# Kernel optimization log

Hardware: AMD Instinct MI355X
Metric: run time of the kernel (lower is better)

## Reference

```python
import jax, jax.numpy as jnp
import numpy as np

CHEB_K = 2  # chebyshev polynomial order (support_ks = [I, A] for cheb_k=2)


def _fc(x, w1, b1, w2, b2, w3, b3):
    # FC module: Linear -> sigmoid -> Linear -> sigmoid -> Linear
    h = jax.nn.sigmoid(x @ w1 + b1)
    h = jax.nn.sigmoid(h @ w2 + b2)
    return h @ w3 + b3


def _preprocess(adj):
    # adj: [B,N,N]; add self-loops then row-normalize
    adj = adj + jnp.eye(adj.shape[-1], dtype=adj.dtype)
    return adj / adj.sum(-1, keepdims=True)


def _gcn(x, adjs, ne, wpool, bpool):
    # x: [B,N,C], adjs: list of [B,N,N], ne: [N,E]
    # wpool: [E, 2*CHEB_K, C, O], bpool: [E, O]
    mats = []
    for A in adjs:
        ks = [jnp.broadcast_to(jnp.eye(A.shape[-1], dtype=A.dtype), A.shape), A]
        for _ in range(2, CHEB_K):
            ks.append(2.0 * jnp.matmul(A, ks[-1]) - ks[-2])
        mats.extend(ks)
    # [B,N,K,C] with K = 2*CHEB_K
    x_g = jnp.stack([jnp.einsum('bnm,bmc->bnc', S, x) for S in mats], axis=2)
    weights = jnp.einsum('nd,dkio->nkio', ne, wpool)  # [N,K,C,O]
    bias = ne @ bpool  # [N,O]
    return jnp.einsum('bnki,nkio->bno', x_g, weights) + bias


def _forward(x, state, ne0, ne1, ne2, fc1_w1, fc1_b1, fc1_w2, fc1_b2, fc1_w3, fc1_b3,
             fc2_w1, fc2_b1, fc2_w2, fc2_b2, fc2_w3, fc2_b3, gate_w, gate_b, upd_w, upd_b):
    hid = upd_w.shape[-1]
    ins = jnp.concatenate([x, state], axis=-1)  # [B,N,dim_in+hid]
    f1 = _fc(ins, fc1_w1, fc1_b1, fc1_w2, fc1_b2, fc1_w3, fc1_b3)  # [B,N,TD]
    f2 = _fc(ins, fc2_w1, fc2_b1, fc2_w2, fc2_b2, fc2_w3, fc2_b3)
    nv1 = jnp.tanh(ne0[:, None, :] * f1)  # einsum 'bd,bnd->bnd' == broadcast mul
    nv2 = jnp.tanh(ne1[:, None, :] * f2)
    adj = jnp.einsum('bnd,bmd->bnm', nv1, nv2) - jnp.einsum('bnd,bmd->bnm', nv2, nv1)
    adj1 = _preprocess(jax.nn.relu(adj))
    adj2 = _preprocess(jax.nn.relu(-jnp.swapaxes(adj, -2, -1)))
    z_r = jax.nn.sigmoid(_gcn(ins, [adj1, adj2], ne2, gate_w, gate_b))
    z, r = z_r[..., :hid], z_r[..., hid:]
    cand = jnp.concatenate([x, z * state], axis=-1)
    hc = jnp.tanh(_gcn(cand, [adj1, adj2], ne2, upd_w, upd_b))
    return r * state + (1.0 - r) * hc


def setup_inputs():
    B, N, DIN, DOUT, ED, TD = 32, 1024, 2, 64, 10, 32
    HG, MID = 16, 2  # hyperGNN_dim, middle_dim hardcoded in FC
    CIN = DIN + DOUT
    K2 = 2 * CHEB_K
    ks = jax.random.split(jax.random.key(0), 16)
    rn = lambda i, shape, s=1.0: jax.random.normal(ks[i], shape, dtype=jnp.float32) * s
    return {
        'x': rn(0, (B, N, DIN)),
        'state': rn(1, (B, N, DOUT)),
        'ne0': rn(2, (B, TD)),
        'ne1': rn(3, (B, TD)),
        'ne2': rn(4, (N, ED), 0.1),
        'fc1_w1': rn(5, (CIN, HG), 0.1), 'fc1_b1': jnp.zeros((HG,), jnp.float32),
        'fc1_w2': rn(6, (HG, MID), 0.1), 'fc1_b2': jnp.zeros((MID,), jnp.float32),
        'fc1_w3': rn(7, (MID, TD), 0.1), 'fc1_b3': jnp.zeros((TD,), jnp.float32),
        'fc2_w1': rn(8, (CIN, HG), 0.1), 'fc2_b1': jnp.zeros((HG,), jnp.float32),
        'fc2_w2': rn(9, (HG, MID), 0.1), 'fc2_b2': jnp.zeros((MID,), jnp.float32),
        'fc2_w3': rn(10, (MID, TD), 0.1), 'fc2_b3': jnp.zeros((TD,), jnp.float32),
        'gate_w': rn(11, (ED, K2, CIN, 2 * DOUT), 0.1),
        'gate_b': rn(12, (ED, 2 * DOUT), 0.1),
        'upd_w': rn(13, (ED, K2, CIN, DOUT), 0.1),
        'upd_b': rn(14, (ED, DOUT), 0.1),
    }


def reference(x, state, ne0, ne1, ne2, fc1_w1, fc1_b1, fc1_w2, fc1_b2, fc1_w3, fc1_b3,
              fc2_w1, fc2_b1, fc2_w2, fc2_b2, fc2_w3, fc2_b3, gate_w, gate_b, upd_w, upd_b):
    return _forward(x, state, ne0, ne1, ne2, fc1_w1, fc1_b1, fc1_w2, fc1_b2, fc1_w3, fc1_b3,
                    fc2_w1, fc2_b1, fc2_w2, fc2_b2, fc2_w3, fc2_b3, gate_w, gate_b, upd_w, upd_b)
```

## Files before the change

kernel.cpp:

```cpp
#include <hip/hip_runtime.h>
#include <math.h>

#define BB   32
#define NN   1024
#define DIN  2
#define DOUT 64
#define CIN  66
#define TD   32
#define ED   10
#define OG   128
#define OU   64
#define KP   160
#define XTR  80

typedef __bf16 bf16x8 __attribute__((ext_vector_type(8)));
typedef float  f32x4  __attribute__((ext_vector_type(4)));
typedef short  s16x8  __attribute__((ext_vector_type(8)));

__device__ __forceinline__ unsigned short f2b(float f) {
    __bf16 h = (__bf16)f;
    return *(unsigned short*)&h;
}

__global__ __launch_bounds__(256) void k_pre(
    const float* __restrict__ x, const float* __restrict__ state,
    const float* __restrict__ ne0, const float* __restrict__ ne1,
    const float* __restrict__ ne2,
    const float* __restrict__ w11, const float* __restrict__ b11,
    const float* __restrict__ w12, const float* __restrict__ b12,
    const float* __restrict__ w13, const float* __restrict__ b13,
    const float* __restrict__ w21, const float* __restrict__ b21,
    const float* __restrict__ w22, const float* __restrict__ b22,
    const float* __restrict__ w23, const float* __restrict__ b23,
    const float* __restrict__ gate_w, const float* __restrict__ gate_b,
    const float* __restrict__ upd_w, const float* __restrict__ upd_b,
    unsigned short* __restrict__ nv1b, unsigned short* __restrict__ nv2b,
    unsigned short* __restrict__ XT0, unsigned short* __restrict__ XT1,
    unsigned short* __restrict__ BcTg, unsigned short* __restrict__ BcTu,
    float* __restrict__ biasG, float* __restrict__ biasU)
{
    __shared__ float sw[2408];
    __shared__ unsigned short st[68*72];
    int blk = blockIdx.x;
    int t = threadIdx.x;

    if (blk < 128) {
        const int oW1 = 0, oB1 = 1056, oW2 = 1072, oB2 = 1104, oW3 = 1108, oB3 = 1172, F2 = 1204;
        for (int i = t; i < 1056; i += 256) { sw[oW1+i] = w11[i]; sw[F2+oW1+i] = w21[i]; }
        if (t < 16) { sw[oB1+t] = b11[t]; sw[F2+oB1+t] = b21[t]; }
        if (t < 32) { sw[oW2+t] = w12[t]; sw[F2+oW2+t] = w22[t]; }
        if (t < 2)  { sw[oB2+t] = b12[t]; sw[F2+oB2+t] = b22[t]; }
        if (t < 64) { sw[oW3+t] = w13[t]; sw[F2+oW3+t] = w23[t]; }
        if (t >= 64 && t < 96) { sw[oB3+t-64] = b13[t-64]; sw[F2+oB3+t-64] = b23[t-64]; }
        __syncthreads();

        int p = blk*256 + t;
        int b = p >> 10;

        float h1a[16], h1b[16];
        #pragma unroll
        for (int j = 0; j < 16; ++j) { h1a[j] = sw[oB1+j]; h1b[j] = sw[F2+oB1+j]; }
        for (int i = 0; i < CIN; ++i) {
            float v = (i < DIN) ? x[(size_t)p*DIN + i] : state[(size_t)p*DOUT + (i-DIN)];
            #pragma unroll
            for (int jq = 0; jq < 4; ++jq) {
                float4 wa = *(const float4*)&sw[oW1 + i*16 + jq*4];
                float4 wb = *(const float4*)&sw[F2 + oW1 + i*16 + jq*4];
                h1a[jq*4+0] += v*wa.x; h1a[jq*4+1] += v*wa.y;
                h1a[jq*4+2] += v*wa.z; h1a[jq*4+3] += v*wa.w;
                h1b[jq*4+0] += v*wb.x; h1b[jq*4+1] += v*wb.y;
                h1b[jq*4+2] += v*wb.z; h1b[jq*4+3] += v*wb.w;
            }
        }
        #pragma unroll
        for (int j = 0; j < 16; ++j) {
            h1a[j] = 1.f/(1.f + __expf(-h1a[j]));
            h1b[j] = 1.f/(1.f + __expf(-h1b[j]));
        }
        float h2a0 = sw[oB2+0], h2a1 = sw[oB2+1];
        float h2b0 = sw[F2+oB2+0], h2b1 = sw[F2+oB2+1];
        #pragma unroll
        for (int i = 0; i < 16; ++i) {
            h2a0 += h1a[i]*sw[oW2 + i*2 + 0];
            h2a1 += h1a[i]*sw[oW2 + i*2 + 1];
            h2b0 += h1b[i]*sw[F2+oW2 + i*2 + 0];
            h2b1 += h1b[i]*sw[F2+oW2 + i*2 + 1];
        }
        h2a0 = 1.f/(1.f + __expf(-h2a0)); h2a1 = 1.f/(1.f + __expf(-h2a1));
        h2b0 = 1.f/(1.f + __expf(-h2b0)); h2b1 = 1.f/(1.f + __expf(-h2b1));

        const float* pn0 = ne0 + b*TD;
        const float* pn1 = ne1 + b*TD;
        #pragma unroll
        for (int jq = 0; jq < 8; ++jq) {
            float4 ba  = *(const float4*)&sw[oB3 + jq*4];
            float4 wa0 = *(const float4*)&sw[oW3 + jq*4];
            float4 wa1 = *(const float4*)&sw[oW3 + 32 + jq*4];
            float4 bb2 = *(const float4*)&sw[F2+oB3 + jq*4];
            float4 wb0 = *(const float4*)&sw[F2+oW3 + jq*4];
            float4 wb1 = *(const float4*)&sw[F2+oW3 + 32 + jq*4];
            float4 n0 = *(const float4*)&pn0[jq*4];
            float4 n1 = *(const float4*)&pn1[jq*4];
            ushort4 u1, u2;
            u1.x = f2b(tanhf(n0.x*(ba.x + h2a0*wa0.x + h2a1*wa1.x)));
            u1.y = f2b(tanhf(n0.y*(ba.y + h2a0*wa0.y + h2a1*wa1.y)));
            u1.z = f2b(tanhf(n0.z*(ba.z + h2a0*wa0.z + h2a1*wa1.z)));
            u1.w = f2b(tanhf(n0.w*(ba.w + h2a0*wa0.w + h2a1*wa1.w)));
            u2.x = f2b(tanhf(n1.x*(bb2.x + h2b0*wb0.x + h2b1*wb1.x)));
            u2.y = f2b(tanhf(n1.y*(bb2.y + h2b0*wb0.y + h2b1*wb1.y)));
            u2.z = f2b(tanhf(n1.z*(bb2.z + h2b0*wb0.z + h2b1*wb1.z)));
            u2.w = f2b(tanhf(n1.w*(bb2.w + h2b0*wb0.w + h2b1*wb1.w)));
            *(ushort4*)&nv1b[(size_t)p*TD + jq*4] = u1;
            *(ushort4*)&nv2b[(size_t)p*TD + jq*4] = u2;
        }
    } else if (blk < 640) {
        int idx = blk - 128;
        int b = idx >> 4, m0 = (idx & 15)*64;
        for (int i = t; i < 1024; i += 256) {
            int m = i >> 4, cq = i & 15;
            size_t base = (size_t)b*NN + m0 + m;
            float4 v = *(const float4*)&state[base*DOUT + cq*4];
            st[(2 + cq*4 + 0)*72 + m] = f2b(v.x);
            st[(2 + cq*4 + 1)*72 + m] = f2b(v.y);
            st[(2 + cq*4 + 2)*72 + m] = f2b(v.z);
            st[(2 + cq*4 + 3)*72 + m] = f2b(v.w);
        }
        if (t < 128) {
            int m = t >> 1, c = t & 1;
            st[c*72 + m] = f2b(x[((size_t)b*NN + m0 + m)*DIN + c]);
        }
        __syncthreads();
        const unsigned int ONE2 = 0x3F803F80u;
        for (int i = t; i < XTR*8; i += 256) {
            int c = i >> 3, ch = i & 7;
            uint4 v;
            if (c < 66)      v = *(const uint4*)&st[c*72 + ch*8];
            else if (c == 66) v = make_uint4(ONE2, ONE2, ONE2, ONE2);
            else              v = make_uint4(0, 0, 0, 0);
            *(uint4*)&XT0[((size_t)b*XTR + c)*NN + m0 + ch*8] = v;
            if (c < 2 || c >= 66)
                *(uint4*)&XT1[((size_t)b*XTR + c)*NN + m0 + ch*8] = v;
        }
    } else if (blk < 1840) {
        int tid = (blk - 640)*256 + t;
        int c = tid / KP, k = tid - c*KP;
        const float* pool; int O, cc; unsigned short* dst;
        if (c < 1280) { pool = gate_w; O = OG; cc = c;        dst = BcTg; }
        else          { pool = upd_w;  O = OU; cc = c - 1280; dst = BcTu; }
        int d = cc / O, o = cc - d*O;
        float v = 0.f;
        if (k < 132) {
            int kp = (k < 66) ? 0 : 1;
            int i  = (k < 66) ? k : k - 66;
            v = pool[(size_t)((d*4 + kp)*CIN + i)*O + o]
              + pool[(size_t)((d*4 + kp + 2)*CIN + i)*O + o];
        }
        dst[(size_t)cc*KP + k] = f2b(v);
    } else {
        int i = (blk - 1840)*256 + t;
        int n = i / 192, j = i - n*192;
        float v = 0.f;
        if (j < 128) {
            #pragma unroll
            for (int d = 0; d < ED; ++d) v += ne2[(size_t)n*ED + d]*gate_b[d*OG + j];
            biasG[(size_t)n*OG + j] = v;
        } else {
            int o = j - 128;
            #pragma unroll
            for (int d = 0; d < ED; ++d) v += ne2[(size_t)n*ED + d]*upd_b[d*OU + o];
            biasU[(size_t)n*OU + o] = v;
        }
    }
}

__global__ __launch_bounds__(256) void k_aapply(
    const unsigned short* __restrict__ nv1b, const unsigned short* __restrict__ nv2b,
    const unsigned short* __restrict__ XTg, unsigned short* __restrict__ A)
{
    __shared__ unsigned short s_nv1r[64*40], s_nv2r[64*40];
    __shared__ unsigned short s_nv1c[64*40], s_nv2c[64*40];
    __shared__ unsigned short s_p[64*72];
    __shared__ unsigned short s_xt[80*72];
    __shared__ float s_rs[64];

    int t = threadIdx.x;
    int b = blockIdx.y, rbase = blockIdx.x*64;
    int w = t >> 6, lane = t & 63, lq = lane >> 4, ln = lane & 15;

    for (int i = t; i < 512; i += 256) {
        int arr = i >> 8, j = i & 255;
        int node = j >> 2, ch = j & 3;
        const unsigned short* src = (arr ? nv2b : nv1b)
            + ((size_t)b*NN + rbase + node)*TD + ch*8;
        unsigned short* dst = (arr ? s_nv2r : s_nv1r) + node*40 + ch*8;
        *(uint4*)dst = *(const uint4*)src;
    }
    __syncthreads();

    bf16x8 a1 = *(const bf16x8*)&s_nv1r[(16*w + ln)*40 + lq*8];
    s16x8 a2s = *(const s16x8*)&s_nv2r[(16*w + ln)*40 + lq*8];
    const s16x8 sgn = {(short)0x8000,(short)0x8000,(short)0x8000,(short)0x8000,
                       (short)0x8000,(short)0x8000,(short)0x8000,(short)0x8000};
    a2s ^= sgn;
    bf16x8 a2n = (bf16x8)a2s;

    f32x4 acc[5];
    #pragma unroll
    for (int i = 0; i < 5; ++i) acc[i] = (f32x4){0.f,0.f,0.f,0.f};
    const f32x4 zero4 = {0.f,0.f,0.f,0.f};

    for (int mb = 0; mb < NN; mb += 64) {
        __syncthreads();
        for (int i = t; i < 512; i += 256) {
            int arr = i >> 8, j = i & 255;
            int node = j >> 2, ch = j & 3;
            const unsigned short* src = (arr ? nv2b : nv1b)
                + ((size_t)b*NN + mb + node)*TD + ch*8;
            unsigned short* dst = (arr ? s_nv2c : s_nv1c) + node*40 + ch*8;
            *(uint4*)dst = *(const uint4*)src;
        }
        for (int i = t; i < 640; i += 256) {
            int c = i >> 3, ch = i & 7;
            *(uint4*)&s_xt[c*72 + ch*8] =
                *(const uint4*)&XTg[((size_t)b*XTR + c)*NN + mb + ch*8];
        }
        __syncthreads();

        #pragma unroll
        for (int j0t = 0; j0t < 4; ++j0t) {
            int j0 = j0t*16;
            bf16x8 b2 = *(const bf16x8*)&s_nv2c[(j0 + ln)*40 + lq*8];
            bf16x8 b1 = *(const bf16x8*)&s_nv1c[(j0 + ln)*40 + lq*8];
            f32x4 s = __builtin_amdgcn_mfma_f32_16x16x32_bf16(a1,  b2, zero4, 0, 0, 0);
            s       = __builtin_amdgcn_mfma_f32_16x16x32_bf16(a2n, b1, s,     0, 0, 0);
            #pragma unroll
            for (int r = 0; r < 4; ++r) {
                float p = fmaxf(s[r], 0.f);
                *(__bf16*)&s_p[(16*w + lq*4 + r)*72 + j0 + ln] = (__bf16)p;
            }
        }

        bf16x8 pa0 = *(const bf16x8*)&s_p[(16*w + ln)*72 +      lq*8];
        bf16x8 pa1 = *(const bf16x8*)&s_p[(16*w + ln)*72 + 32 + lq*8];
        #pragma unroll
        for (int n0t = 0; n0t < 5; ++n0t) {
            int n0 = n0t*16;
            bf16x8 xb0 = *(const bf16x8*)&s_xt[(n0 + ln)*72 +      lq*8];
            bf16x8 xb1 = *(const bf16x8*)&s_xt[(n0 + ln)*72 + 32 + lq*8];
            acc[n0t] = __builtin_amdgcn_mfma_f32_16x16x32_bf16(pa0, xb0, acc[n0t], 0, 0, 0);
            acc[n0t] = __builtin_amdgcn_mfma_f32_16x16x32_bf16(pa1, xb1, acc[n0t], 0, 0, 0);
        }
    }

    if (ln == 2) {
        #pragma unroll
        for (int r = 0; r < 4; ++r) s_rs[16*w + lq*4 + r] = acc[4][r];
    }
    float rinv[4];
    #pragma unroll
    for (int r = 0; r < 4; ++r) rinv[r] = 1.0f / (1.0f + s_rs[16*w + lq*4 + r]);

    #pragma unroll
    for (int n0t = 0; n0t < 5; ++n0t) {
        int c = n0t*16 + ln;
        if (c < CIN) {
            #pragma unroll
            for (int r = 0; r < 4; ++r) {
                int gr = rbase + 16*w + lq*4 + r;
                size_t rowG = (size_t)b*NN + gr;
                unsigned short xu = XTg[((size_t)b*XTR + c)*NN + gr];
                float xr = (float)(*(const __bf16*)&xu);
                A[rowG*KP + c]      = xu;
                A[rowG*KP + 66 + c] = f2b((acc[n0t][r] + xr) * rinv[r]);
            }
        }
    }
    for (int i = t; i < 64*28; i += 256) {
        int rr = i / 28, cc = 132 + (i - 28*(i/28));
        A[((size_t)b*NN + rbase + rr)*KP + cc] = 0;
    }
}

template<int O, int MODE>
__global__ __launch_bounds__(256) void k_gemm(
    const unsigned short* __restrict__ A, const unsigned short* __restrict__ BcT,
    const float* __restrict__ ne2, const float* __restrict__ biasP,
    const float* __restrict__ state, unsigned short* __restrict__ XT1,
    float* __restrict__ rbuf, float* __restrict__ out)
{
    __shared__ unsigned short s_b[160*168];
    __shared__ float s_ne[128*16];

    int t = threadIdx.x;
    int w = t >> 6, lane = t & 63, lq = lane >> 4, ln = lane & 15;
    int o0 = blockIdx.y*16;
    int rowBlock = blockIdx.x*128;

    for (int i = t; i < 3200; i += 256) {
        int cc = i / 20, kc = i - cc*20;
        int d = cc >> 4, oo = cc & 15;
        *(uint4*)&s_b[cc*168 + kc*8] =
            *(const uint4*)&BcT[(size_t)(d*O + o0 + oo)*KP + kc*8];
    }
    for (int i = t; i < 1280; i += 256) {
        int r = i / 10, d = i - r*10;
        int n = (rowBlock + r) & (NN - 1);
        s_ne[r*16 + d] = ne2[(size_t)n*ED + d];
    }
    __syncthreads();

    int rowW = rowBlock + w*32;
    f32x4 acc0[10], acc1[10];
    #pragma unroll
    for (int i = 0; i < 10; ++i) {
        acc0[i] = (f32x4){0.f,0.f,0.f,0.f};
        acc1[i] = (f32x4){0.f,0.f,0.f,0.f};
    }

    #pragma unroll
    for (int kc = 0; kc < 5; ++kc) {
        bf16x8 af0 = *(const bf16x8*)&A[(size_t)(rowW      + ln)*KP + kc*32 + lq*8];
        bf16x8 af1 = *(const bf16x8*)&A[(size_t)(rowW + 16 + ln)*KP + kc*32 + lq*8];
        #pragma unroll
        for (int ct = 0; ct < 10; ++ct) {
            bf16x8 bf = *(const bf16x8*)&s_b[(ct*16 + ln)*168 + kc*32 + lq*8];
            acc0[ct] = __builtin_amdgcn_mfma_f32_16x16x32_bf16(af0, bf, acc0[ct], 0, 0, 0);
            acc1[ct] = __builtin_amdgcn_mfma_f32_16x16x32_bf16(af1, bf, acc1[ct], 0, 0, 0);
        }
    }

    int o = o0 + ln;
    #pragma unroll
    for (int f = 0; f < 2; ++f) {
        #pragma unroll
        for (int r = 0; r < 4; ++r) {
            int row_l = w*32 + 16*f + lq*4 + r;
            size_t rowG = (size_t)rowBlock + row_l;
            int n = (int)(rowG & (NN - 1));
            int bb = (int)(rowG >> 10);
            f32x4 nA = *(const f32x4*)&s_ne[row_l*16];
            f32x4 nB = *(const f32x4*)&s_ne[row_l*16 + 4];
            float n8 = s_ne[row_l*16 + 8], n9 = s_ne[row_l*16 + 9];
            float val = biasP[(size_t)n*O + o];
            if (f == 0) {
                val += nA.x*acc0[0][r] + nA.y*acc0[1][r] + nA.z*acc0[2][r] + nA.w*acc0[3][r]
                     + nB.x*acc0[4][r] + nB.y*acc0[5][r] + nB.z*acc0[6][r] + nB.w*acc0[7][r]
                     + n8*acc0[8][r] + n9*acc0[9][r];
            } else {
                val += nA.x*acc1[0][r] + nA.y*acc1[1][r] + nA.z*acc1[2][r] + nA.w*acc1[3][r]
                     + nB.x*acc1[4][r] + nB.y*acc1[5][r] + nB.z*acc1[6][r] + nB.w*acc1[7][r]
                     + n8*acc1[8][r] + n9*acc1[9][r];
            }
            if (MODE == 0) {
                float sv = 1.f/(1.f + __expf(-val));
                if (o0 < 64) {
                    float zst = sv * state[rowG*DOUT + o];
                    XT1[((size_t)bb*XTR + 2 + o)*NN + n] = f2b(zst);
                } else {
                    rbuf[rowG*DOUT + (o - 64)] = sv;
                }
            } else {
                float hc = tanhf(val);
                float rg = rbuf[rowG*DOUT + o];
                float st = state[rowG*DOUT + o];
                out[rowG*DOUT + o] = rg*st + (1.f - rg)*hc;
            }
        }
    }
}

extern "C" void kernel_launch(void* const* d_in, const int* in_sizes, int n_in,
                              void* d_out, int out_size, void* d_ws, size_t ws_size,
                              hipStream_t stream)
{
    const float* x      = (const float*)d_in[0];
    const float* state  = (const float*)d_in[1];
    const float* ne0    = (const float*)d_in[2];
    const float* ne1    = (const float*)d_in[3];
    const float* ne2    = (const float*)d_in[4];
    const float* f1w1   = (const float*)d_in[5];
    const float* f1b1   = (const float*)d_in[6];
    const float* f1w2   = (const float*)d_in[7];
    const float* f1b2   = (const float*)d_in[8];
    const float* f1w3   = (const float*)d_in[9];
    const float* f1b3   = (const float*)d_in[10];
    const float* f2w1   = (const float*)d_in[11];
    const float* f2b1   = (const float*)d_in[12];
    const float* f2w2   = (const float*)d_in[13];
    const float* f2b2   = (const float*)d_in[14];
    const float* f2w3   = (const float*)d_in[15];
    const float* f2b3   = (const float*)d_in[16];
    const float* gate_w = (const float*)d_in[17];
    const float* gate_b = (const float*)d_in[18];
    const float* upd_w  = (const float*)d_in[19];
    const float* upd_b  = (const float*)d_in[20];

    unsigned short* nv1b = (unsigned short*)d_ws;
    unsigned short* nv2b = nv1b + (size_t)BB*NN*TD;
    unsigned short* XT0  = nv2b + (size_t)BB*NN*TD;
    unsigned short* XT1  = XT0  + (size_t)BB*XTR*NN;
    unsigned short* A    = XT1  + (size_t)BB*XTR*NN;
    unsigned short* BcTg = A    + (size_t)BB*NN*KP;
    unsigned short* BcTu = BcTg + (size_t)1280*KP;
    float* biasG = (float*)(BcTu + (size_t)640*KP);
    float* biasU = biasG + (size_t)NN*OG;
    float* rbuf  = biasU + (size_t)NN*OU;
    float* out   = (float*)d_out;

    k_pre<<<dim3(2608), 256, 0, stream>>>(x, state, ne0, ne1, ne2,
        f1w1, f1b1, f1w2, f1b2, f1w3, f1b3,
        f2w1, f2b1, f2w2, f2b2, f2w3, f2b3,
        gate_w, gate_b, upd_w, upd_b,
        nv1b, nv2b, XT0, XT1, BcTg, BcTu, biasG, biasU);

    k_aapply<<<dim3(NN/64, BB), 256, 0, stream>>>(nv1b, nv2b, XT0, A);

    k_gemm<OG,0><<<dim3(BB*NN/128, 8), 256, 0, stream>>>(A, BcTg, ne2, biasG,
                                                         state, XT1, rbuf, nullptr);

    k_aapply<<<dim3(NN/64, BB), 256, 0, stream>>>(nv1b, nv2b, XT1, A);

    k_gemm<OU,1><<<dim3(BB*NN/128, 4), 256, 0, stream>>>(A, BcTu, ne2, biasU,
                                                         state, nullptr, rbuf, out);
}
```

Baseline: 273.2 us.

## Halve GEMM shared B tile, pad P scratch stride, remap aapply block order

The GEMM kernel now stages the per-embedding-dim weight slab in two halves of 5 dims each, cutting its shared memory from about 54KB to about 27KB. It also drops the ne2 shared cache and reads ne2 directly from global memory in the epilogue, so more blocks can be resident per CU. The price is an extra barrier and a serialized second load phase. The aapply kernel pads its P scratch row stride from 72 to 88 to reduce LDS bank conflicts. It also flattens its grid so consecutive blocks walk the batch dimension first, which changes L2 locality of the XT and nv reads.

Result: faster. 255.0 us (-6.7%).

```diff
diff --git a/kernel.cpp b/kernel.cpp
--- a/kernel.cpp
+++ b/kernel.cpp
@@ -12,6 +12,7 @@
 #define OU   64
 #define KP   160
 #define XTR  80
+#define PS   88
 
 typedef __bf16 bf16x8 __attribute__((ext_vector_type(8)));
 typedef float  f32x4  __attribute__((ext_vector_type(4)));
@@ -179,12 +180,13 @@
 {
     __shared__ unsigned short s_nv1r[64*40], s_nv2r[64*40];
     __shared__ unsigned short s_nv1c[64*40], s_nv2c[64*40];
-    __shared__ unsigned short s_p[64*72];
+    __shared__ unsigned short s_p[64*PS];
     __shared__ unsigned short s_xt[80*72];
     __shared__ float s_rs[64];
 
     int t = threadIdx.x;
-    int b = blockIdx.y, rbase = blockIdx.x*64;
+    int id = blockIdx.x;
+    int b = id & 31, rbase = (id >> 5)*64;
     int w = t >> 6, lane = t & 63, lq = lane >> 4, ln = lane & 15;
 
     for (int i = t; i < 512; i += 256) {
@@ -236,12 +238,12 @@
             #pragma unroll
             for (int r = 0; r < 4; ++r) {
                 float p = fmaxf(s[r], 0.f);
-                *(__bf16*)&s_p[(16*w + lq*4 + r)*72 + j0 + ln] = (__bf16)p;
+                *(__bf16*)&s_p[(16*w + lq*4 + r)*PS + j0 + ln] = (__bf16)p;
             }
         }
 
-        bf16x8 pa0 = *(const bf16x8*)&s_p[(16*w + ln)*72 +      lq*8];
-        bf16x8 pa1 = *(const bf16x8*)&s_p[(16*w + ln)*72 + 32 + lq*8];
+        bf16x8 pa0 = *(const bf16x8*)&s_p[(16*w + ln)*PS +      lq*8];
+        bf16x8 pa1 = *(const bf16x8*)&s_p[(16*w + ln)*PS + 32 + lq*8];
         #pragma unroll
         for (int n0t = 0; n0t < 5; ++n0t) {
             int n0 = n0t*16;
@@ -288,44 +290,43 @@
     const float* __restrict__ state, unsigned short* __restrict__ XT1,
     float* __restrict__ rbuf, float* __restrict__ out)
 {
-    __shared__ unsigned short s_b[160*168];
-    __shared__ float s_ne[128*16];
+    __shared__ unsigned short s_b[80*168];
 
     int t = threadIdx.x;
     int w = t >> 6, lane = t & 63, lq = lane >> 4, ln = lane & 15;
     int o0 = blockIdx.y*16;
     int rowBlock = blockIdx.x*128;
-
-    for (int i = t; i < 3200; i += 256) {
-        int cc = i / 20, kc = i - cc*20;
-        int d = cc >> 4, oo = cc & 15;
-        *(uint4*)&s_b[cc*168 + kc*8] =
-            *(const uint4*)&BcT[(size_t)(d*O + o0 + oo)*KP + kc*8];
-    }
-    for (int i = t; i < 1280; i += 256) {
-        int r = i / 10, d = i - r*10;
-        int n = (rowBlock + r) & (NN - 1);
-        s_ne[r*16 + d] = ne2[(size_t)n*ED + d];
-    }
-    __syncthreads();
-
     int rowW = rowBlock + w*32;
-    f32x4 acc0[10], acc1[10];
-    #pragma unroll
-    for (int i = 0; i < 10; ++i) {
-        acc0[i] = (f32x4){0.f,0.f,0.f,0.f};
-        acc1[i] = (f32x4){0.f,0.f,0.f,0.f};
-    }
-
-    #pragma unroll
-    for (int kc = 0; kc < 5; ++kc) {
-        bf16x8 af0 = *(const bf16x8*)&A[(size_t)(rowW      + ln)*KP + kc*32 + lq*8];
-        bf16x8 af1 = *(const bf16x8*)&A[(size_t)(rowW + 16 + ln)*KP + kc*32 + lq*8];
-        #pragma unroll
-        for (int ct = 0; ct < 10; ++ct) {
-            bf16x8 bf = *(const bf16x8*)&s_b[(ct*16 + ln)*168 + kc*32 + lq*8];
-            acc0[ct] = __builtin_amdgcn_mfma_f32_16x16x32_bf16(af0, bf, acc0[ct], 0, 0, 0);
-            acc1[ct] = __builtin_amdgcn_mfma_f32_16x16x32_bf16(af1, bf, acc1[ct], 0, 0, 0);
+
+    f32x4 acc[2][2][5];
+    #pragma unroll
+    for (int h = 0; h < 2; ++h)
+        #pragma unroll
+        for (int f = 0; f < 2; ++f)
+            #pragma unroll
+            for (int c = 0; c < 5; ++c) acc[h][f][c] = (f32x4){0.f,0.f,0.f,0.f};
+
+    #pragma unroll
+    for (int h = 0; h < 2; ++h) {
+        if (h) __syncthreads();
+        for (int i = t; i < 1600; i += 256) {
+            int cc = i / 20, kc = i - cc*20;
+            int d = h*5 + (cc >> 4), oo = cc & 15;
+            *(uint4*)&s_b[cc*168 + kc*8] =
+                *(const uint4*)&BcT[(size_t)(d*O + o0 + oo)*KP + kc*8];
+        }
+        __syncthreads();
+
+        #pragma unroll
+        for (int kc = 0; kc < 5; ++kc) {
+            bf16x8 af0 = *(const bf16x8*)&A[(size_t)(rowW      + ln)*KP + kc*32 + lq*8];
+            bf16x8 af1 = *(const bf16x8*)&A[(size_t)(rowW + 16 + ln)*KP + kc*32 + lq*8];
+            #pragma unroll
+            for (int ct = 0; ct < 5; ++ct) {
+                bf16x8 bf = *(const bf16x8*)&s_b[(ct*16 + ln)*168 + kc*32 + lq*8];
+                acc[h][0][ct] = __builtin_amdgcn_mfma_f32_16x16x32_bf16(af0, bf, acc[h][0][ct], 0, 0, 0);
+                acc[h][1][ct] = __builtin_amdgcn_mfma_f32_16x16x32_bf16(af1, bf, acc[h][1][ct], 0, 0, 0);
+            }
         }
     }
 
@@ -338,19 +339,12 @@
             size_t rowG = (size_t)rowBlock + row_l;
             int n = (int)(rowG & (NN - 1));
             int bb = (int)(rowG >> 10);
-            f32x4 nA = *(const f32x4*)&s_ne[row_l*16];
-            f32x4 nB = *(const f32x4*)&s_ne[row_l*16 + 4];
-            float n8 = s_ne[row_l*16 + 8], n9 = s_ne[row_l*16 + 9];
+            const float* nep = &ne2[(size_t)n*ED];
             float val = biasP[(size_t)n*O + o];
-            if (f == 0) {
-                val += nA.x*acc0[0][r] + nA.y*acc0[1][r] + nA.z*acc0[2][r] + nA.w*acc0[3][r]
-                     + nB.x*acc0[4][r] + nB.y*acc0[5][r] + nB.z*acc0[6][r] + nB.w*acc0[7][r]
-                     + n8*acc0[8][r] + n9*acc0[9][r];
-            } else {
-                val += nA.x*acc1[0][r] + nA.y*acc1[1][r] + nA.z*acc1[2][r] + nA.w*acc1[3][r]
-                     + nB.x*acc1[4][r] + nB.y*acc1[5][r] + nB.z*acc1[6][r] + nB.w*acc1[7][r]
-                     + n8*acc1[8][r] + n9*acc1[9][r];
-            }
+            #pragma unroll
+            for (int d = 0; d < 5; ++d) val += nep[d]     * acc[0][f][d][r];
+            #pragma unroll
+            for (int d = 0; d < 5; ++d) val += nep[5 + d] * acc[1][f][d][r];
             if (MODE == 0) {
                 float sv = 1.f/(1.f + __expf(-val));
                 if (o0 < 64) {
@@ -413,12 +407,12 @@
         gate_w, gate_b, upd_w, upd_b,
         nv1b, nv2b, XT0, XT1, BcTg, BcTu, biasG, biasU);
 
-    k_aapply<<<dim3(NN/64, BB), 256, 0, stream>>>(nv1b, nv2b, XT0, A);
+    k_aapply<<<dim3(512), 256, 0, stream>>>(nv1b, nv2b, XT0, A);
 
     k_gemm<OG,0><<<dim3(BB*NN/128, 8), 256, 0, stream>>>(A, BcTg, ne2, biasG,
                                                          state, XT1, rbuf, nullptr);
 
-    k_aapply<<<dim3(NN/64, BB), 256, 0, stream>>>(nv1b, nv2b, XT1, A);
+    k_aapply<<<dim3(512), 256, 0, stream>>>(nv1b, nv2b, XT1, A);
 
     k_gemm<OU,1><<<dim3(BB*NN/128, 4), 256, 0, stream>>>(A, BcTu, ne2, biasU,
                                                          state, nullptr, rbuf, out);
```
